# Kernel optimization log

Measured on AMD Instinct MI355X. Metric: run time of the kernel, lower is better.

## Reference

```python
import jax, jax.numpy as jnp
import numpy as np
from jax import lax

V = 50000          # vocab
E = 64             # embedding_dim
B = 64             # batch
SEQ = 1024         # sentence length
NC = 6             # num_classes
L = 4              # num_layers (total conv layers)
KTOP = 4
NF = [10, 14, 18, 22]          # num_filters per stage
KS = [7, 5, 5, 3]              # kernel sizes
ROWS = [E // 2**i for i in range(5)]   # [64,32,16,8,4]
GROUPS = ROWS[:4]              # conv_i groups = rows[i-1]
# dynamic k-max schedule: k_l = max(k_top, ceil((L-l)/L * SEQ)) for l=1,2,3; last pool uses k_top
KPOOL = [max(KTOP, int(np.ceil((L - l) / L * SEQ))) for l in (1, 2, 3)] + [KTOP]  # [768,512,256,4]


def _uniform(key, shape, fan):
    s = 1.0 / np.sqrt(fan)
    return jax.random.uniform(key, shape, jnp.float32, -s, s)


def setup_inputs() -> dict:
    key = jax.random.key(0)
    ks = jax.random.split(key, 16)
    tokens = jax.random.randint(ks[0], (B, SEQ), 0, V)
    emb = jax.random.normal(ks[1], (V, E), jnp.float32)
    inp = {"tokens": tokens, "emb": emb}
    # conv weights: OIH layout, I = in_channels / groups = num_filters[i-1] (or 1 for conv1)
    in_pg = [1, NF[0], NF[1], NF[2]]
    out_ch = [NF[i] * ROWS[i] for i in range(4)]   # [640,448,288,176]
    for i in range(4):
        fan = in_pg[i] * KS[i]
        inp[f"w{i+1}"] = _uniform(ks[2 + 2 * i], (out_ch[i], in_pg[i], KS[i]), fan)
        inp[f"b{i+1}"] = _uniform(ks[3 + 2 * i], (out_ch[i],), fan)
    fc_in = ROWS[4] * NF[3] * KTOP   # 4*22*4 = 352
    inp["fcw"] = _uniform(ks[10], (NC, fc_in), fc_in)
    inp["fcb"] = _uniform(ks[11], (NC,), fc_in)
    return inp


def _fold(x, nf):
    # channel index c = row*nf + filt; sum adjacent rows pairwise (Fold(2,2))
    b, d, s = x.shape
    r = d // nf
    return x.reshape(b, r // 2, 2, nf, s).sum(axis=2).reshape(b, d // 2, s)


def _kmax(x, k):
    # top-k along seq axis, preserving original temporal order
    _, idx = lax.top_k(x, k)
    idx = jnp.sort(idx, axis=-1)
    return jnp.take_along_axis(x, idx, axis=-1)


def reference(tokens, emb, w1, b1, w2, b2, w3, b3, w4, b4, fcw, fcb):
    x = emb[tokens]                 # (B, S, E)
    x = x.transpose(0, 2, 1)        # (B, E, S)
    ws, bs = (w1, w2, w3, w4), (b1, b2, b3, b4)
    for i in range(4):
        pad = KS[i] - 1             # 'wide' convolution
        x = lax.conv_general_dilated(
            x, ws[i], (1,), [(pad, pad)],
            dimension_numbers=("NCH", "OIH", "NCH"),
            feature_group_count=GROUPS[i],
        ) + bs[i][None, :, None]
        x = _fold(x, NF[i])
        x = _kmax(x, KPOOL[i])
        x = jnp.tanh(x)
    # dropout is identity in eval mode
    x = x.reshape(x.shape[0], -1)   # (B, 352)
    return x @ fcw.T + fcb
```

## Files before the change

kernel.cpp:

```cpp
#include <hip/hip_runtime.h>
#include <hip/hip_bf16.h>
#include <math.h>


#if defined(__has_builtin)
#if __has_builtin(__builtin_amdgcn_ballot_w64)
#define BALLOT64(expr) __builtin_amdgcn_ballot_w64(expr)
#endif
#endif
#ifndef BALLOT64
#define BALLOT64(expr) __ballot(expr)
#endif

__device__ __forceinline__ unsigned f2ord(float f) {
    unsigned u = __float_as_uint(f);
    return (u & 0x80000000u) ? ~u : (u | 0x80000000u);
}
__device__ __forceinline__ float ord2f(unsigned key) {
    unsigned u = (key & 0x80000000u) ? (key & 0x7fffffffu) : ~key;
    return __uint_as_float(u);
}
__device__ __forceinline__ float tanh_fast(float x) {
    float e = __expf(2.f * x);
    return 1.f - 2.f * __builtin_amdgcn_rcpf(e + 1.f);
}
__device__ __forceinline__ int mbcnt64(unsigned long long m) {
    return __builtin_amdgcn_mbcnt_hi((unsigned)(m >> 32),
           __builtin_amdgcn_mbcnt_lo((unsigned)m, 0u));
}

template<int CH>
__device__ __forceinline__ void select_finish(const unsigned* keys, unsigned T,
                                              int k, float* stage,
                                              float* __restrict__ out)
{
    int g = 0, e = 0;
    #pragma unroll
    for (int i = 0; i < CH; ++i) { g += (keys[i] > T); e += (keys[i] == T); }

    int gtBefore = 0, eqBefore = 0, totG = 0;
    #pragma unroll
    for (int b = 0; b < 5; ++b) {
        unsigned long long mg = BALLOT64((((g >> b) & 1) != 0));
        unsigned long long me = BALLOT64((((e >> b) & 1) != 0));
        gtBefore += mbcnt64(mg) << b;
        eqBefore += mbcnt64(me) << b;
        totG     += __popcll(mg) << b;
    }
    const int needTies = k - totG;

    int gRun = 0, eRun = 0;
    #pragma unroll
    for (int i = 0; i < CH; ++i) {
        const unsigned key = keys[i];
        const bool isG = key > T;
        const bool isE = key == T;
        const int eIdx = eqBefore + eRun;
        const int dst = gtBefore + gRun + min(eIdx, needTies);
        if (isG || (isE && eIdx < needTies))
            stage[dst] = tanh_fast(ord2f(key));
        gRun += isG; eRun += isE;
    }
    const int lane = threadIdx.x & 63;
    for (int i = lane; i < k; i += 64)
        out[i] = stage[i];
}

template<int N, int CH>
__device__ void wave_selectN(const unsigned (*keys)[CH], int k, float* stage,
                             float* const* outs)
{
    unsigned p[N];
    int above[N], buck[N];
    #pragma unroll
    for (int n = 0; n < N; ++n) { p[n] = 0u; above[n] = 0; buck[n] = 64 * CH; }

    unsigned doneMask = 0;
    const unsigned allDone = (1u << N) - 1u;
    #pragma unroll 1
    for (int pos = 31; pos >= 0; --pos) {
        #pragma unroll
        for (int n = 0; n < N; ++n) {
            if (!((doneMask >> n) & 1u)) {
                const unsigned t = p[n] | (1u << pos);
                int c = 0;
                #pragma unroll
                for (int i = 0; i < CH; ++i)
                    c += __popcll(BALLOT64((keys[n][i] >= t)));
                const int inb = c - above[n];
                const int rem = k - above[n];
                if (inb >= rem) { p[n] = t; buck[n] = inb; }
                else            { above[n] += inb; buck[n] -= inb; }
                if (buck[n] == k - above[n]) doneMask |= (1u << n);
            }
        }
        if (doneMask == allDone) break;
    }
    #pragma unroll
    for (int n = 0; n < N; ++n)
        select_finish<CH>(keys[n], p[n], k, stage, outs[n]);
}

__global__ __launch_bounds__(128) void layer1_fused(
    const int* __restrict__ tokens, const float* __restrict__ emb,
    const float* __restrict__ W1, const float* __restrict__ B1,
    float* __restrict__ Z1)
{
    const int j = blockIdx.x;
    const int b = blockIdx.y;
    const int t = threadIdx.x;
    const int w = t >> 6;
    const int lane = t & 63;

    __shared__ float xr[2][1100];
    __shared__ float stagebuf[2][768];

    const float2* emb2 = (const float2*)emb;
    for (int i = t; i < 1100; i += 128) {
        int s = i - 6;
        float a = 0.f, c = 0.f;
        if (s >= 0 && s < 1024) {
            int tok = tokens[b * 1024 + s];
            float2 v = emb2[(size_t)tok * 32 + j];
            a = v.x; c = v.y;
        }
        xr[0][i] = a;
        xr[1][i] = c;
    }
    __syncthreads();

    const int beg = lane * 17;

    unsigned keys[5][17];
    float* outs[5];
    const size_t orow = (size_t)b * 320 + (size_t)j * 10;

    #pragma unroll
    for (int q = 0; q < 5; ++q) {
        const int f = 5 * w + q;
        float wa[7], wb[7];
        #pragma unroll
        for (int k2 = 0; k2 < 7; ++k2) {
            wa[k2] = W1[(2 * j * 10 + f) * 7 + k2];
            wb[k2] = W1[((2 * j + 1) * 10 + f) * 7 + k2];
        }
        const float bias = B1[2 * j * 10 + f] + B1[(2 * j + 1) * 10 + f];
        #pragma unroll
        for (int i = 0; i < 17; ++i) {
            float acc = bias;
            #pragma unroll
            for (int k2 = 0; k2 < 7; ++k2)
                acc += xr[0][beg + i + k2] * wa[k2]
                     + xr[1][beg + i + k2] * wb[k2];
            keys[q][i] = (beg + i < 1030) ? f2ord(acc) : 0u;
        }
        outs[q] = Z1 + (orow + f) * 768;
    }
    wave_selectN<5, 17>(keys, 768, stagebuf[w], outs);
}

template <int IPG, int NF, int K, int SIN, int SOUT, int KSEL, int NW, int CH,
          int PHASES>
__global__ __launch_bounds__(NW * 64) void conv_fold_select_kernel(
    const float* __restrict__ X, const float* __restrict__ W,
    const float* __restrict__ Bias, float* __restrict__ Z,
    int Cin, int Cfold)
{
    static_assert(NF == 2 * NW, "2 filters per wave");
    static_assert(64 * CH >= SOUT, "chunk covers row");
    constexpr int W2 = 64 * CH + K - 1;
    constexpr int RS = 2 * IPG / PHASES;

    const int t = threadIdx.x;
    const int j = blockIdx.x;
    const int b = blockIdx.y;
    const int wav = t >> 6, lane = t & 63;

    __shared__ float xs[RS][W2];
    __shared__ float stagebuf[NW][KSEL];

    const float* Xb = X + ((size_t)b * Cin + (size_t)(2 * j) * IPG) * SIN;

    const int f0 = __builtin_amdgcn_readfirstlane(2 * wav);
    float acc0[CH], acc1[CH];
    {
        float bias0 = Bias[2 * j * NF + f0]     + Bias[(2 * j + 1) * NF + f0];
        float bias1 = Bias[2 * j * NF + f0 + 1] + Bias[(2 * j + 1) * NF + f0 + 1];
        #pragma unroll
        for (int i = 0; i < CH; ++i) { acc0[i] = bias0; acc1[i] = bias1; }
    }
    const int base = lane * CH;

    #pragma unroll 1
    for (int ph = 0; ph < PHASES; ++ph) {
        if (ph) __syncthreads();
        for (int idx = t; idx < RS * W2; idx += NW * 64) {
            int r = idx / W2, p = idx - r * W2;
            int sg = p - (K - 1);
            int gr = ph * RS + r;
            xs[r][p] = (sg >= 0 && sg < SIN) ? Xb[(size_t)gr * SIN + sg] : 0.f;
        }
        __syncthreads();

        int h = (ph * RS) / IPG, c = (ph * RS) % IPG;
        #pragma unroll 1
        for (int r = 0; r < RS; ++r) {
            float win[CH + K - 1];
            #pragma unroll
            for (int p = 0; p < CH + K - 1; ++p)
                win[p] = xs[r][base + p];
            const float* Wp = W + ((size_t)((2 * j + h) * NF + f0) * IPG + c) * K;
            #pragma unroll
            for (int k2 = 0; k2 < K; ++k2) {
                const float w0 = Wp[k2];
                const float w1 = Wp[(size_t)IPG * K + k2];
                #pragma unroll
                for (int i = 0; i < CH; ++i) {
                    acc0[i] = fmaf(win[i + k2], w0, acc0[i]);
                    acc1[i] = fmaf(win[i + k2], w1, acc1[i]);
                }
            }
            if (++c == IPG) { c = 0; ++h; }
        }
    }

    unsigned keys[2][CH];
    #pragma unroll
    for (int i = 0; i < CH; ++i) {
        keys[0][i] = (base + i < SOUT) ? f2ord(acc0[i]) : 0u;
        keys[1][i] = (base + i < SOUT) ? f2ord(acc1[i]) : 0u;
    }
    const size_t orow = (size_t)b * Cfold + (size_t)j * NF;
    float* outs[2] = { Z + (orow + f0) * (size_t)KSEL,
                       Z + (orow + f0 + 1) * (size_t)KSEL };
    wave_selectN<2, CH>(keys, KSEL, stagebuf[wav], outs);
}

__global__ __launch_bounds__(192) void fc_kernel(
    const float* __restrict__ Z, const float* __restrict__ Wf,
    const float* __restrict__ bf, float* __restrict__ out)
{
    int g = blockIdx.x * blockDim.x + threadIdx.x;
    if (g >= 64 * 6) return;
    int b = g / 6, c = g % 6;
    float acc = bf[c];
    const float* zr = Z + b * 352;
    const float* wr = Wf + c * 352;
    for (int i = 0; i < 352; ++i) acc += zr[i] * wr[i];
    out[g] = acc;
}

extern "C" void kernel_launch(void* const* d_in, const int* in_sizes, int n_in,
                              void* d_out, int out_size, void* d_ws, size_t ws_size,
                              hipStream_t stream)
{
    const int*   tokens = (const int*)  d_in[0];
    const float* emb    = (const float*)d_in[1];
    const float* w1     = (const float*)d_in[2];
    const float* b1     = (const float*)d_in[3];
    const float* w2     = (const float*)d_in[4];
    const float* b2     = (const float*)d_in[5];
    const float* w3     = (const float*)d_in[6];
    const float* b3     = (const float*)d_in[7];
    const float* w4     = (const float*)d_in[8];
    const float* b4     = (const float*)d_in[9];
    const float* fcw    = (const float*)d_in[10];
    const float* fcb    = (const float*)d_in[11];
    float* out = (float*)d_out;
    float* ws  = (float*)d_ws;

    float* Z1 = ws;
    float* Z2 = ws + 15728640;
    float* Z3 = ws;
    float* Z4 = ws + 2359296;

    layer1_fused<<<dim3(32, 64), 128, 0, stream>>>(tokens, emb, w1, b1, Z1);

    conv_fold_select_kernel<10, 14, 5, 768, 772, 512, 7, 13, 2>
        <<<dim3(16, 64), 7 * 64, 0, stream>>>(Z1, w2, b2, Z2, 320, 224);

    conv_fold_select_kernel<14, 18, 5, 512, 516, 256, 9, 9, 1>
        <<<dim3(8, 64), 9 * 64, 0, stream>>>(Z2, w3, b3, Z3, 224, 144);

    conv_fold_select_kernel<18, 22, 3, 256, 258, 4, 11, 5, 1>
        <<<dim3(4, 64), 11 * 64, 0, stream>>>(Z3, w4, b4, Z4, 144, 88);

    fc_kernel<<<2, 192, 0, stream>>>(Z4, fcw, fcb, out);
}
```

Measured before the change: 343.8 us.

## Fuse layer-1 and layer-2 conv/fold/kmax into one kernel via shared memory

Merges the embedding+conv1+fold+kmax kernel with the conv2 stage so each block computes both groups' layer-1 rows directly into shared memory and then convolves them, never writing the large Z1 intermediate to global memory. It uses 14 waves per block, one per layer-2 filter, with 10 of them doing the layer-1 selections, and it vectorises the final stage-to-global copy with float4. This removes a large global write and read of Z1 and one launch. In exchange it needs more shared memory, serialises work across phases with barriers, and leaves some waves idle during layer 1.

```diff
diff --git a/kernel.cpp b/kernel.cpp
--- a/kernel.cpp
+++ b/kernel.cpp
@@ -29,7 +29,7 @@
            __builtin_amdgcn_mbcnt_lo((unsigned)m, 0u));
 }
 
-template<int CH>
+template<int CH, bool COPY>
 __device__ __forceinline__ void select_finish(const unsigned* keys, unsigned T,
                                               int k, float* stage,
                                               float* __restrict__ out)
@@ -61,14 +61,41 @@
             stage[dst] = tanh_fast(ord2f(key));
         gRun += isG; eRun += isE;
     }
-    const int lane = threadIdx.x & 63;
-    for (int i = lane; i < k; i += 64)
-        out[i] = stage[i];
+    if (COPY) {
+        const int lane = threadIdx.x & 63;
+        const float4* s4 = (const float4*)stage;
+        float4* o4 = (float4*)out;
+        #pragma unroll 1
+        for (int i = lane; i < (k >> 2); i += 64)
+            o4[i] = s4[i];
+    }
+}
+
+template<int CH, bool COPY>
+__device__ void wave_select1(const unsigned* keys, int k, float* stage,
+                             float* __restrict__ out)
+{
+    unsigned p = 0u;
+    int above = 0, buck = 64 * CH;
+    #pragma unroll 1
+    for (int pos = 31; pos >= 0; --pos) {
+        const unsigned t = p | (1u << pos);
+        int c = 0;
+        #pragma unroll
+        for (int i = 0; i < CH; ++i)
+            c += __popcll(BALLOT64((keys[i] >= t)));
+        const int inb = c - above;
+        const int rem = k - above;
+        if (inb >= rem) { p = t; buck = inb; }
+        else            { above += inb; buck -= inb; }
+        if (buck == k - above) break;
+    }
+    select_finish<CH, COPY>(keys, p, k, stage, out);
 }
 
 template<int N, int CH>
-__device__ void wave_selectN(const unsigned (*keys)[CH], int k, float* stage,
-                             float* const* outs)
+__device__ void wave_selectN_ballot(const unsigned (*keys)[CH], int k,
+                                    float* stage, float* const* outs)
 {
     unsigned p[N];
     int above[N], buck[N];
@@ -98,65 +125,119 @@
     }
     #pragma unroll
     for (int n = 0; n < N; ++n)
-        select_finish<CH>(keys[n], p[n], k, stage, outs[n]);
-}
-
-__global__ __launch_bounds__(128) void layer1_fused(
+        select_finish<CH, true>(keys[n], p[n], k, stage, outs[n]);
+}
+
+__global__ __launch_bounds__(896) void layer12_fused(
     const int* __restrict__ tokens, const float* __restrict__ emb,
     const float* __restrict__ W1, const float* __restrict__ B1,
-    float* __restrict__ Z1)
-{
-    const int j = blockIdx.x;
-    const int b = blockIdx.y;
-    const int t = threadIdx.x;
-    const int w = t >> 6;
+    const float* __restrict__ W2, const float* __restrict__ B2,
+    float* __restrict__ Z2)
+{
+    const int j2 = blockIdx.x;
+    const int b  = blockIdx.y;
+    const int t  = threadIdx.x;
+    const int wav  = t >> 6;
     const int lane = t & 63;
 
-    __shared__ float xr[2][1100];
-    __shared__ float stagebuf[2][768];
-
+    __shared__ __align__(16) float z1[10][836];
+    __shared__ __align__(16) float uni[14 * 512];
+    float (*xr)[1100] = reinterpret_cast<float (*)[1100]>(uni);
     const float2* emb2 = (const float2*)emb;
-    for (int i = t; i < 1100; i += 128) {
-        int s = i - 6;
-        float a = 0.f, c = 0.f;
-        if (s >= 0 && s < 1024) {
-            int tok = tokens[b * 1024 + s];
-            float2 v = emb2[(size_t)tok * 32 + j];
-            a = v.x; c = v.y;
-        }
-        xr[0][i] = a;
-        xr[1][i] = c;
+
+    for (int i = t; i < 10 * 836; i += 896) ((float*)z1)[i] = 0.f;
+
+    const int f = __builtin_amdgcn_readfirstlane(wav);
+    float acc[13];
+    {
+        const float bias = B2[(2 * j2) * 14 + f] + B2[(2 * j2 + 1) * 14 + f];
+        #pragma unroll
+        for (int i = 0; i < 13; ++i) acc[i] = bias;
+    }
+    const int base = lane * 13;
+
+    {
+        const int g = 2 * j2;
+        for (int i = t; i < 1100; i += 896) {
+            int s = i - 6; float a = 0.f, c = 0.f;
+            if (s >= 0 && s < 1024) {
+                int tok = tokens[b * 1024 + s];
+                float2 v = emb2[(size_t)tok * 32 + g];
+                a = v.x; c = v.y;
+            }
+            xr[0][i] = a; xr[1][i] = c;
+        }
     }
     __syncthreads();
 
-    const int beg = lane * 17;
-
-    unsigned keys[5][17];
-    float* outs[5];
-    const size_t orow = (size_t)b * 320 + (size_t)j * 10;
-
-    #pragma unroll
-    for (int q = 0; q < 5; ++q) {
-        const int f = 5 * w + q;
-        float wa[7], wb[7];
-        #pragma unroll
-        for (int k2 = 0; k2 < 7; ++k2) {
-            wa[k2] = W1[(2 * j * 10 + f) * 7 + k2];
-            wb[k2] = W1[((2 * j + 1) * 10 + f) * 7 + k2];
-        }
-        const float bias = B1[2 * j * 10 + f] + B1[(2 * j + 1) * 10 + f];
-        #pragma unroll
-        for (int i = 0; i < 17; ++i) {
-            float acc = bias;
+    #pragma unroll 1
+    for (int ph = 0; ph < 2; ++ph) {
+        const int g = 2 * j2 + ph;
+
+        if (wav < 10) {
+            const int f1 = wav;
+            float wa[7], wb[7];
             #pragma unroll
-            for (int k2 = 0; k2 < 7; ++k2)
-                acc += xr[0][beg + i + k2] * wa[k2]
-                     + xr[1][beg + i + k2] * wb[k2];
-            keys[q][i] = (beg + i < 1030) ? f2ord(acc) : 0u;
-        }
-        outs[q] = Z1 + (orow + f) * 768;
-    }
-    wave_selectN<5, 17>(keys, 768, stagebuf[w], outs);
+            for (int k2 = 0; k2 < 7; ++k2) {
+                wa[k2] = W1[(2 * g * 10 + f1) * 7 + k2];
+                wb[k2] = W1[((2 * g + 1) * 10 + f1) * 7 + k2];
+            }
+            const float bias1 = B1[2 * g * 10 + f1] + B1[(2 * g + 1) * 10 + f1];
+            const int beg = lane * 17;
+            unsigned keys1[17];
+            #pragma unroll
+            for (int i = 0; i < 17; ++i) {
+                float a1 = bias1;
+                #pragma unroll
+                for (int k2 = 0; k2 < 7; ++k2)
+                    a1 += xr[0][beg + i + k2] * wa[k2]
+                        + xr[1][beg + i + k2] * wb[k2];
+                keys1[i] = (beg + i < 1030) ? f2ord(a1) : 0u;
+            }
+            wave_select1<17, false>(keys1, 768, &z1[wav][4], nullptr);
+        }
+        __syncthreads();
+
+        if (ph == 0) {
+            const int g1 = 2 * j2 + 1;
+            for (int i = t; i < 1100; i += 896) {
+                int s = i - 6; float a = 0.f, c = 0.f;
+                if (s >= 0 && s < 1024) {
+                    int tok = tokens[b * 1024 + s];
+                    float2 v = emb2[(size_t)tok * 32 + g1];
+                    a = v.x; c = v.y;
+                }
+                xr[0][i] = a; xr[1][i] = c;
+            }
+        }
+
+        {
+            const float* Wp0 = W2 + (size_t)((2 * j2 + ph) * 14 + f) * 10 * 5;
+            #pragma unroll 1
+            for (int r = 0; r < 10; ++r) {
+                float win[17];
+                #pragma unroll
+                for (int p = 0; p < 17; ++p) win[p] = z1[r][base + p];
+                const float* Wp = Wp0 + r * 5;
+                #pragma unroll
+                for (int k2 = 0; k2 < 5; ++k2) {
+                    const float w0 = Wp[k2];
+                    #pragma unroll
+                    for (int i = 0; i < 13; ++i)
+                        acc[i] = fmaf(win[i + k2], w0, acc[i]);
+                }
+            }
+        }
+        if (ph == 0) __syncthreads();
+    }
+
+    unsigned keys2[13];
+    #pragma unroll
+    for (int i = 0; i < 13; ++i)
+        keys2[i] = (base + i < 772) ? f2ord(acc[i]) : 0u;
+    float* stage = uni + wav * 512;
+    float* outp = Z2 + ((size_t)b * 224 + (size_t)j2 * 14 + f) * 512;
+    wave_select1<13, true>(keys2, 512, stage, outp);
 }
 
 template <int IPG, int NF, int K, int SIN, int SOUT, int KSEL, int NW, int CH,
@@ -176,8 +257,8 @@
     const int b = blockIdx.y;
     const int wav = t >> 6, lane = t & 63;
 
-    __shared__ float xs[RS][W2];
-    __shared__ float stagebuf[NW][KSEL];
+    __shared__ __align__(16) float xs[RS][W2];
+    __shared__ __align__(16) float stagebuf[NW][KSEL];
 
     const float* Xb = X + ((size_t)b * Cin + (size_t)(2 * j) * IPG) * SIN;
 
@@ -233,7 +314,7 @@
     const size_t orow = (size_t)b * Cfold + (size_t)j * NF;
     float* outs[2] = { Z + (orow + f0) * (size_t)KSEL,
                        Z + (orow + f0 + 1) * (size_t)KSEL };
-    wave_selectN<2, CH>(keys, KSEL, stagebuf[wav], outs);
+    wave_selectN_ballot<2, CH>(keys, KSEL, stagebuf[wav], outs);
 }
 
 __global__ __launch_bounds__(192) void fc_kernel(
@@ -269,15 +350,12 @@
     float* out = (float*)d_out;
     float* ws  = (float*)d_ws;
 
-    float* Z1 = ws;
     float* Z2 = ws + 15728640;
     float* Z3 = ws;
     float* Z4 = ws + 2359296;
 
-    layer1_fused<<<dim3(32, 64), 128, 0, stream>>>(tokens, emb, w1, b1, Z1);
-
-    conv_fold_select_kernel<10, 14, 5, 768, 772, 512, 7, 13, 2>
-        <<<dim3(16, 64), 7 * 64, 0, stream>>>(Z1, w2, b2, Z2, 320, 224);
+    layer12_fused<<<dim3(16, 64), 896, 0, stream>>>(
+        tokens, emb, w1, b1, w2, b2, Z2);
 
     conv_fold_select_kernel<14, 18, 5, 512, 516, 256, 9, 9, 1>
         <<<dim3(8, 64), 9 * 64, 0, stream>>>(Z2, w3, b3, Z3, 224, 144);
```

Measured after the change: 331.0 us. -3.7%, faster.
